# Kernel tuning notes

Measured on AMD Instinct MI355X. Metric: run time of the kernel, lower is better.

Reference implementation:

```python
import jax, jax.numpy as jnp
import numpy as np

CHNN = 1024
K = 2048


def _conv1x1(W, b, x):
    # x: (B, C_in, L), W: (C_out, C_in), b: (C_out,)
    return jnp.einsum('oc,bcl->bol', W, x) + b[None, :, None]


def setup_inputs() -> dict:
    key = jax.random.key(0)
    ks = jax.random.split(key, 10)
    s = 0.02
    return {
        'vc': jax.random.normal(ks[0], (1, CHNN, K), dtype=jnp.float32),
        'vm': jax.random.normal(ks[1], (1, CHNN, K), dtype=jnp.float32),
        'W_ak': jax.random.normal(ks[2], (K, CHNN), dtype=jnp.float32) * s,
        'b_ak': jax.random.normal(ks[3], (K,), dtype=jnp.float32) * s,
        'W_c': jax.random.normal(ks[4], (CHNN, CHNN), dtype=jnp.float32) * s,
        'b_c': jax.random.normal(ks[5], (CHNN,), dtype=jnp.float32) * s,
        'W_mad': jax.random.normal(ks[6], (CHNN, CHNN), dtype=jnp.float32) * s,
        'b_mad': jax.random.normal(ks[7], (CHNN,), dtype=jnp.float32) * s,
        'W_gcn': jax.random.normal(ks[8], (CHNN, CHNN), dtype=jnp.float32) * s,
        'b_gcn': jax.random.normal(ks[9], (CHNN,), dtype=jnp.float32) * s,
    }


def reference(vc, vm, W_ak, b_ak, W_c, b_c, W_mad, b_mad, W_gcn, b_gcn):
    # vcw: (1, K, L) assignment logits; softmax over the K (channel) dim
    vcw = _conv1x1(W_ak, b_ak, vc)
    vcw = jax.nn.softmax(vcw, axis=1)
    w = vcw[0].T                      # (L, K)  (batch forced to 1 by squeeze(0))
    # vm features: (1, CHNN, K)
    vmr = jax.nn.relu(_conv1x1(W_c, b_c, vm))
    # F.linear(vm, w): contract last dim (K) with w's second dim -> (1, CHNN, L)
    vma = jnp.einsum('bck,lk->bcl', vmr, w)
    vma = _conv1x1(W_mad, b_mad, vma)  # (1, CHNN, L)
    # dense adjacency over positions: (1, L, L)
    A = jnp.einsum('bck,bcl->bkl', vma, vma)
    # GCN: x (1, K, CHNN) @ W + b, then softmax(A) @ x  (requires L == K)
    x = jnp.swapaxes(vmr, 1, 2) @ W_gcn + b_gcn
    A = jax.nn.softmax(A, axis=-1)
    out = A @ x                        # (1, L, CHNN)
    return jnp.swapaxes(out, 1, 2)     # (1, CHNN, L)
```

## Files before the change

### kernel.cpp

```cpp
#include <hip/hip_runtime.h>
#include <hip/hip_bf16.h>


typedef __bf16 bf16x4 __attribute__((ext_vector_type(4)));
typedef __bf16 bf16x8 __attribute__((ext_vector_type(8)));
typedef float  f32x4  __attribute__((ext_vector_type(4)));

typedef const void __attribute__((address_space(1)))* gptr_t;
typedef void       __attribute__((address_space(3)))* lptr_t;

__device__ __forceinline__ void load16_lds(const __bf16* g, __bf16* l)
{
    __builtin_amdgcn_global_load_lds((gptr_t)g, (lptr_t)l, 16, 0, 0);
}

#define WAITCNT_VM8 0x0F78
#define WAITCNT_VM0 0x0F70

template<typename OT, int BIAS_, bool RELU_, int STORE_>
struct GC {
    using OUT_T = OT;
    static constexpr int BIAS = BIAS_, STORE = STORE_;
    static constexpr bool RELU = RELU_;
};

template<class CF>
__device__ __forceinline__ void gemm_body(
    int bid, __bf16* sA, __bf16* sB,
    const __bf16* __restrict__ A, const __bf16* __restrict__ B,
    const float* __restrict__ bias,
    typename CF::OUT_T* __restrict__ C, typename CF::OUT_T* __restrict__ CT,
    int M, int N, int K, int ntx)
{
    const int lane = threadIdx.x & 63;
    const int m0 = (bid / ntx) * 64, n0 = (bid % ntx) * 64;
    const __bf16* gA = A + (size_t)m0 * K;
    const __bf16* gB = B + (size_t)n0 * K;

    f32x4 acc[4][4];
    #pragma unroll
    for (int i = 0; i < 4; ++i)
        #pragma unroll
        for (int j = 0; j < 4; ++j)
            acc[i][j] = (f32x4){0.f, 0.f, 0.f, 0.f};

    auto stage = [&](int k0, int buf) {
        #pragma unroll
        for (int i = 0; i < 4; ++i) {
            const int c = i * 64 + lane;
            load16_lds(gA + (size_t)(c >> 2) * K + k0 + (c & 3) * 8,
                       &sA[buf * 2048 + i * 512]);
        }
        #pragma unroll
        for (int i = 0; i < 4; ++i) {
            const int c = i * 64 + lane;
            load16_lds(gB + (size_t)(c >> 2) * K + k0 + (c & 3) * 8,
                       &sB[buf * 2048 + i * 512]);
        }
    };

    stage(0, 0);
    stage(32, 1);
    int cur = 0;
    for (int k0 = 0; k0 < K - 32; k0 += 32) {
        __builtin_amdgcn_s_waitcnt(WAITCNT_VM8);
        bf16x8 af[4], bfr[4];
        #pragma unroll
        for (int i = 0; i < 4; ++i) {
            af[i]  = *(const bf16x8*)&sA[cur * 2048 + (i * 16 + (lane & 15)) * 32 + (lane >> 4) * 8];
            bfr[i] = *(const bf16x8*)&sB[cur * 2048 + (i * 16 + (lane & 15)) * 32 + (lane >> 4) * 8];
        }
        #pragma unroll
        for (int i = 0; i < 4; ++i)
            #pragma unroll
            for (int j = 0; j < 4; ++j)
                acc[i][j] = __builtin_amdgcn_mfma_f32_16x16x32_bf16(af[i], bfr[j], acc[i][j], 0, 0, 0);
        if (k0 + 64 < K) stage(k0 + 64, cur);
        cur ^= 1;
    }
    __builtin_amdgcn_s_waitcnt(WAITCNT_VM0);
    {
        bf16x8 af[4], bfr[4];
        #pragma unroll
        for (int i = 0; i < 4; ++i) {
            af[i]  = *(const bf16x8*)&sA[cur * 2048 + (i * 16 + (lane & 15)) * 32 + (lane >> 4) * 8];
            bfr[i] = *(const bf16x8*)&sB[cur * 2048 + (i * 16 + (lane & 15)) * 32 + (lane >> 4) * 8];
        }
        #pragma unroll
        for (int i = 0; i < 4; ++i)
            #pragma unroll
            for (int j = 0; j < 4; ++j)
                acc[i][j] = __builtin_amdgcn_mfma_f32_16x16x32_bf16(af[i], bfr[j], acc[i][j], 0, 0, 0);
    }

    #pragma unroll
    for (int i = 0; i < 4; ++i) {
        const int rowb = m0 + i * 16 + (lane >> 4) * 4;
        #pragma unroll
        for (int j = 0; j < 4; ++j) {
            const int col = n0 + j * 16 + (lane & 15);
            f32x4 v = acc[i][j];
            #pragma unroll
            for (int r = 0; r < 4; ++r) {
                float f = v[r];
                if (CF::BIAS == 1) f += bias[rowb + r];
                if (CF::BIAS == 2) f += bias[col];
                if (CF::RELU) f = fmaxf(f, 0.f);
                v[r] = f;
            }
            if (CF::STORE == 0) {
                #pragma unroll
                for (int r = 0; r < 4; ++r)
                    C[(size_t)(rowb + r) * N + col] = (typename CF::OUT_T)v[r];
            } else {
                if constexpr (sizeof(typename CF::OUT_T) == 4) {
                    *(f32x4*)&CT[(size_t)col * M + rowb] = v;
                } else {
                    bf16x4 w = { (__bf16)v[0], (__bf16)v[1], (__bf16)v[2], (__bf16)v[3] };
                    *(bf16x4*)&CT[(size_t)col * M + rowb] = w;
                }
            }
        }
    }
}

__device__ __forceinline__ void softmax_row_w(__bf16* __restrict__ p)
{
    const int lane = threadIdx.x & 63;
    bf16x8 v[4];
    float f[32];
    #pragma unroll
    for (int r = 0; r < 4; ++r)
        v[r] = *(const bf16x8*)&p[(r * 64 + lane) * 8];
    float m = -1e30f;
    #pragma unroll
    for (int r = 0; r < 4; ++r)
        #pragma unroll
        for (int j = 0; j < 8; ++j) {
            f[r * 8 + j] = (float)v[r][j];
            m = fmaxf(m, f[r * 8 + j]);
        }
    #pragma unroll
    for (int s = 1; s < 64; s <<= 1) m = fmaxf(m, __shfl_xor(m, s, 64));
    float sum = 0.f;
    #pragma unroll
    for (int i = 0; i < 32; ++i) { f[i] = expf(f[i] - m); sum += f[i]; }
    #pragma unroll
    for (int s = 1; s < 64; s <<= 1) sum += __shfl_xor(sum, s, 64);
    const float inv = 1.f / sum;
    #pragma unroll
    for (int r = 0; r < 4; ++r) {
        bf16x8 w;
        #pragma unroll
        for (int j = 0; j < 8; ++j) w[j] = (__bf16)(f[r * 8 + j] * inv);
        *(bf16x8*)&p[(r * 64 + lane) * 8] = w;
    }
}

template<class CF>
__global__ __launch_bounds__(64, 2)
void gemm1w(const __bf16* __restrict__ A, const __bf16* __restrict__ B,
            const float* __restrict__ bias,
            typename CF::OUT_T* __restrict__ C, typename CF::OUT_T* __restrict__ CT,
            int M, int N, int K, int ntx)
{
    __shared__ __bf16 sAB[8192];
    gemm_body<CF>(blockIdx.x, sAB, sAB + 4096, A, B, bias, C, CT, M, N, K, ntx);
}

template<class C1, class C2>
__global__ __launch_bounds__(64, 2)
void gemm2w(int nblk1,
            const __bf16* __restrict__ A1, const __bf16* __restrict__ B1,
            const float* __restrict__ b1,
            typename C1::OUT_T* __restrict__ C1p, typename C1::OUT_T* __restrict__ CT1,
            int M1, int N1, int K1, int ntx1,
            const __bf16* __restrict__ A2, const __bf16* __restrict__ B2,
            const float* __restrict__ b2,
            typename C2::OUT_T* __restrict__ C2p, typename C2::OUT_T* __restrict__ CT2,
            int M2, int N2, int K2, int ntx2)
{
    __shared__ __bf16 sAB[8192];
    const int b = blockIdx.x;
    if (b < nblk1)
        gemm_body<C1>(b, sAB, sAB + 4096, A1, B1, b1, C1p, CT1, M1, N1, K1, ntx1);
    else
        gemm_body<C2>(b - nblk1, sAB, sAB + 4096, A2, B2, b2, C2p, CT2, M2, N2, K2, ntx2);
}

template<class C1, class C2>
__global__ __launch_bounds__(64, 2)
void gemm2smw(int nblk1, int nblk2,
              const __bf16* __restrict__ A1, const __bf16* __restrict__ B1,
              const float* __restrict__ b1, typename C1::OUT_T* __restrict__ C1p,
              int M1, int N1, int K1, int ntx1,
              const __bf16* __restrict__ A2, const __bf16* __restrict__ B2,
              const float* __restrict__ b2, typename C2::OUT_T* __restrict__ C2p,
              int M2, int N2, int K2, int ntx2,
              __bf16* __restrict__ SM)
{
    __shared__ __bf16 sAB[8192];
    const int b = blockIdx.x;
    if (b < nblk1)
        gemm_body<C1>(b, sAB, sAB + 4096, A1, B1, b1, C1p,
                      (typename C1::OUT_T*)nullptr, M1, N1, K1, ntx1);
    else if (b < nblk1 + nblk2)
        gemm_body<C2>(b - nblk1, sAB, sAB + 4096, A2, B2, b2, C2p,
                      (typename C2::OUT_T*)nullptr, M2, N2, K2, ntx2);
    else
        softmax_row_w(SM + (size_t)(b - nblk1 - nblk2) * 2048);
}

__global__ __launch_bounds__(64)
void row_softmax_w(__bf16* __restrict__ A)
{
    softmax_row_w(A + (size_t)blockIdx.x * 2048);
}

__device__ __forceinline__ void tp_tile(const float* __restrict__ in,
                                        __bf16* __restrict__ outp,
                                        int R, int C, int bx, int by)
{
    __shared__ float t[32][33];
    const int tx = threadIdx.x & 31, ty = threadIdx.x >> 5;
    #pragma unroll
    for (int i = ty; i < 32; i += 8)
        t[i][tx] = in[(size_t)(by + i) * C + (bx + tx)];
    __syncthreads();
    #pragma unroll
    for (int i = ty; i < 32; i += 8)
        outp[(size_t)(bx + i) * R + (by + tx)] = (__bf16)t[tx][i];
}

__device__ __forceinline__ void cast_blk(const float* __restrict__ s,
                                         __bf16* __restrict__ d, int blk)
{
    const int i = blk * 1024 + threadIdx.x * 4;
    float4 v = *(const float4*)&s[i];
    bf16x4 w = { (__bf16)v.x, (__bf16)v.y, (__bf16)v.z, (__bf16)v.w };
    *(bf16x4*)&d[i] = w;
}

__global__ __launch_bounds__(256)
void prep(const float* __restrict__ vc, __bf16* __restrict__ vcT,
          const float* __restrict__ vm, __bf16* __restrict__ vmT,
          const float* __restrict__ W_ak, __bf16* __restrict__ W_akb,
          const float* __restrict__ W_c, __bf16* __restrict__ W_cb,
          const float* __restrict__ W_mad, __bf16* __restrict__ W_madb,
          const float* __restrict__ W_gcn, __bf16* __restrict__ W_gcnT)
{
    const int x = blockIdx.x;
    if (blockIdx.z == 0) {
        const float* in = (x < 2048) ? vc : vm;
        __bf16* o       = (x < 2048) ? vcT : vmT;
        const int e = x & 2047;
        tp_tile(in, o, 1024, 2048, (e & 63) * 32, (e >> 6) * 32);
    } else if (blockIdx.z == 1) {
        if (x < 2048)      cast_blk(W_ak, W_akb, x);
        else if (x < 3072) cast_blk(W_c, W_cb, x - 2048);
        else               cast_blk(W_mad, W_madb, x - 3072);
    } else {
        if (x >= 1024) return;
        tp_tile(W_gcn, W_gcnT, 1024, 1024, (x & 31) * 32, (x >> 5) * 32);
    }
}

extern "C" void kernel_launch(void* const* d_in, const int* in_sizes, int n_in,
                              void* d_out, int out_size, void* d_ws, size_t ws_size,
                              hipStream_t stream)
{
    const float* vc    = (const float*)d_in[0];
    const float* vm    = (const float*)d_in[1];
    const float* W_ak  = (const float*)d_in[2];
    const float* b_ak  = (const float*)d_in[3];
    const float* W_c   = (const float*)d_in[4];
    const float* b_c   = (const float*)d_in[5];
    const float* W_mad = (const float*)d_in[6];
    const float* b_mad = (const float*)d_in[7];
    const float* W_gcn = (const float*)d_in[8];
    const float* b_gcn = (const float*)d_in[9];
    float* out = (float*)d_out;

    char* ws = (char*)d_ws;
    const size_t MB = 1u << 20;
    __bf16* ST     = (__bf16*)(ws);
    __bf16* P      = (__bf16*)(ws);
    __bf16* vcT    = (__bf16*)(ws + 8 * MB);
    __bf16* vmaT   = (__bf16*)(ws + 8 * MB);
    __bf16* W_akb  = (__bf16*)(ws + 12 * MB);
    __bf16* vmm    = (__bf16*)(ws + 12 * MB);
    __bf16* vmT    = (__bf16*)(ws + 16 * MB);
    __bf16* xT     = (__bf16*)(ws + 16 * MB);
    __bf16* W_cb   = (__bf16*)(ws + 20 * MB);
    __bf16* W_madb = (__bf16*)(ws + 22 * MB);
    __bf16* vmrT   = (__bf16*)(ws + 24 * MB);
    __bf16* W_gcnT = (__bf16*)(ws + 28 * MB);

    using G3  = GC<__bf16, 2, false, 0>;
    using G5  = GC<__bf16, 1, true,  1>;
    using G6  = GC<__bf16, 0, false, 0>;
    using G11 = GC<__bf16, 1, false, 0>;
    using G7  = GC<__bf16, 2, false, 0>;
    using G9  = GC<__bf16, 0, false, 0>;
    using G12 = GC<float,  0, false, 1>;

    prep<<<dim3(4096, 1, 3), 256, 0, stream>>>(vc, vcT, vm, vmT, W_ak, W_akb,
                                               W_c, W_cb, W_mad, W_madb,
                                               W_gcn, W_gcnT);
    gemm2w<G3, G5><<<1536, 64, 0, stream>>>(1024,
        vcT, W_akb, b_ak, ST, (__bf16*)nullptr, 2048, 2048, 1024, 32,
        W_cb, vmT, b_c, (__bf16*)nullptr, vmrT, 1024, 2048, 1024, 32);
    gemm2smw<G6, G11><<<3072, 64, 0, stream>>>(512, 512,
        W_madb, vmrT, nullptr, vmm, 1024, 2048, 1024, 32,
        W_gcnT, vmrT, b_gcn, xT, 1024, 2048, 1024, 32,
        ST);
    gemm1w<G7><<<512, 64, 0, stream>>>(ST, vmm, b_mad, vmaT, (__bf16*)nullptr,
                                       2048, 1024, 2048, 16);
    gemm1w<G9><<<1024, 64, 0, stream>>>(vmaT, vmaT, nullptr, P, (__bf16*)nullptr,
                                        2048, 2048, 1024, 32);
    row_softmax_w<<<2048, 64, 0, stream>>>(P);
    gemm1w<G12><<<512, 64, 0, stream>>>(P, xT, nullptr, (float*)nullptr, out,
                                        2048, 1024, 2048, 16);
}
```

Baseline: 212.9 us.

## Triple-buffer GEMM LDS staging and XOR-swizzle K chunks to cut bank conflicts

```diff
diff --git a/kernel.cpp b/kernel.cpp
--- a/kernel.cpp
+++ b/kernel.cpp
@@ -14,8 +14,9 @@
     __builtin_amdgcn_global_load_lds((gptr_t)g, (lptr_t)l, 16, 0, 0);
 }
 
-#define WAITCNT_VM8 0x0F78
-#define WAITCNT_VM0 0x0F70
+#define WAITCNT_VM16 0x4F70
+#define WAITCNT_VM8  0x0F78
+#define WAITCNT_VM0  0x0F70
 
 template<typename OT, int BIAS_, bool RELU_, int STORE_>
 struct GC {
@@ -48,50 +49,52 @@
         #pragma unroll
         for (int i = 0; i < 4; ++i) {
             const int c = i * 64 + lane;
-            load16_lds(gA + (size_t)(c >> 2) * K + k0 + (c & 3) * 8,
+            const int s = (c ^ (c >> 2) ^ (c >> 4)) & 3;
+            load16_lds(gA + (size_t)(c >> 2) * K + k0 + s * 8,
                        &sA[buf * 2048 + i * 512]);
         }
         #pragma unroll
         for (int i = 0; i < 4; ++i) {
             const int c = i * 64 + lane;
-            load16_lds(gB + (size_t)(c >> 2) * K + k0 + (c & 3) * 8,
+            const int s = (c ^ (c >> 2) ^ (c >> 4)) & 3;
+            load16_lds(gB + (size_t)(c >> 2) * K + k0 + s * 8,
                        &sB[buf * 2048 + i * 512]);
         }
     };
 
-    stage(0, 0);
-    stage(32, 1);
-    int cur = 0;
-    for (int k0 = 0; k0 < K - 32; k0 += 32) {
-        __builtin_amdgcn_s_waitcnt(WAITCNT_VM8);
+    const int fsw = ((lane >> 4) ^ lane ^ (lane >> 2)) & 3;
+
+    auto compute = [&](int buf) {
         bf16x8 af[4], bfr[4];
         #pragma unroll
         for (int i = 0; i < 4; ++i) {
-            af[i]  = *(const bf16x8*)&sA[cur * 2048 + (i * 16 + (lane & 15)) * 32 + (lane >> 4) * 8];
-            bfr[i] = *(const bf16x8*)&sB[cur * 2048 + (i * 16 + (lane & 15)) * 32 + (lane >> 4) * 8];
+            const int off = buf * 2048 + (i * 16 + (lane & 15)) * 32 + fsw * 8;
+            af[i]  = *(const bf16x8*)&sA[off];
+            bfr[i] = *(const bf16x8*)&sB[off];
         }
         #pragma unroll
         for (int i = 0; i < 4; ++i)
             #pragma unroll
             for (int j = 0; j < 4; ++j)
                 acc[i][j] = __builtin_amdgcn_mfma_f32_16x16x32_bf16(af[i], bfr[j], acc[i][j], 0, 0, 0);
-        if (k0 + 64 < K) stage(k0 + 64, cur);
-        cur ^= 1;
+    };
+
+    stage(0, 0);
+    stage(32, 1);
+    stage(64, 2);
+    int cur = 0;
+    for (int k0 = 0; k0 < K - 96; k0 += 32) {
+        __builtin_amdgcn_s_waitcnt(WAITCNT_VM16);
+        compute(cur);
+        stage(k0 + 96, cur);
+        cur = (cur == 2) ? 0 : cur + 1;
     }
+    __builtin_amdgcn_s_waitcnt(WAITCNT_VM16);
+    compute(cur); cur = (cur == 2) ? 0 : cur + 1;
+    __builtin_amdgcn_s_waitcnt(WAITCNT_VM8);
+    compute(cur); cur = (cur == 2) ? 0 : cur + 1;
     __builtin_amdgcn_s_waitcnt(WAITCNT_VM0);
-    {
-        bf16x8 af[4], bfr[4];
-        #pragma unroll
-        for (int i = 0; i < 4; ++i) {
-            af[i]  = *(const bf16x8*)&sA[cur * 2048 + (i * 16 + (lane & 15)) * 32 + (lane >> 4) * 8];
-            bfr[i] = *(const bf16x8*)&sB[cur * 2048 + (i * 16 + (lane & 15)) * 32 + (lane >> 4) * 8];
-        }
-        #pragma unroll
-        for (int i = 0; i < 4; ++i)
-            #pragma unroll
-            for (int j = 0; j < 4; ++j)
-                acc[i][j] = __builtin_amdgcn_mfma_f32_16x16x32_bf16(af[i], bfr[j], acc[i][j], 0, 0, 0);
-    }
+    compute(cur);
 
     #pragma unroll
     for (int i = 0; i < 4; ++i) {
@@ -164,8 +167,8 @@
             typename CF::OUT_T* __restrict__ C, typename CF::OUT_T* __restrict__ CT,
             int M, int N, int K, int ntx)
 {
-    __shared__ __bf16 sAB[8192];
-    gemm_body<CF>(blockIdx.x, sAB, sAB + 4096, A, B, bias, C, CT, M, N, K, ntx);
+    __shared__ __bf16 sAB[12288];
+    gemm_body<CF>(blockIdx.x, sAB, sAB + 6144, A, B, bias, C, CT, M, N, K, ntx);
 }
 
 template<class C1, class C2>
@@ -180,12 +183,12 @@
             typename C2::OUT_T* __restrict__ C2p, typename C2::OUT_T* __restrict__ CT2,
             int M2, int N2, int K2, int ntx2)
 {
-    __shared__ __bf16 sAB[8192];
+    __shared__ __bf16 sAB[12288];
     const int b = blockIdx.x;
     if (b < nblk1)
-        gemm_body<C1>(b, sAB, sAB + 4096, A1, B1, b1, C1p, CT1, M1, N1, K1, ntx1);
+        gemm_body<C1>(b, sAB, sAB + 6144, A1, B1, b1, C1p, CT1, M1, N1, K1, ntx1);
     else
-        gemm_body<C2>(b - nblk1, sAB, sAB + 4096, A2, B2, b2, C2p, CT2, M2, N2, K2, ntx2);
+        gemm_body<C2>(b - nblk1, sAB, sAB + 6144, A2, B2, b2, C2p, CT2, M2, N2, K2, ntx2);
 }
 
 template<class C1, class C2>
@@ -199,13 +202,13 @@
               int M2, int N2, int K2, int ntx2,
               __bf16* __restrict__ SM)
 {
-    __shared__ __bf16 sAB[8192];
+    __shared__ __bf16 sAB[12288];
     const int b = blockIdx.x;
     if (b < nblk1)
-        gemm_body<C1>(b, sAB, sAB + 4096, A1, B1, b1, C1p,
+        gemm_body<C1>(b, sAB, sAB + 6144, A1, B1, b1, C1p,
                       (typename C1::OUT_T*)nullptr, M1, N1, K1, ntx1);
     else if (b < nblk1 + nblk2)
-        gemm_body<C2>(b - nblk1, sAB, sAB + 4096, A2, B2, b2, C2p,
+        gemm_body<C2>(b - nblk1, sAB, sAB + 6144, A2, B2, b2, C2p,
                       (typename C2::OUT_T*)nullptr, M2, N2, K2, ntx2);
     else
         softmax_row_w(SM + (size_t)(b - nblk1 - nblk2) * 2048);
```

New measurement: 198.5 us. -6.7%, faster.
